# Kernel optimization log

Measured on AMD Instinct MI355X. Metric: run time of the kernel, lower is better.

The kernel has to match this reference:

```python
import jax, jax.numpy as jnp
import numpy as np

LN_EPS = 1e-5

def _layernorm(x, g, b):
    mu = jnp.mean(x, axis=-1, keepdims=True)
    var = jnp.mean(jnp.square(x - mu), axis=-1, keepdims=True)
    return (x - mu) * jax.lax.rsqrt(var + LN_EPS) * g + b

def setup_inputs() -> dict:
    key = jax.random.key(0)
    ks = jax.random.split(key, 12)
    B, S, E = 8, 4096, 512
    H, DK = 64, 8          # d_k = E // H = 8 qubits per head
    NQ_FFN, FFN = 8, 2048
    TWO_PI = 2.0 * np.pi
    x = jax.random.normal(ks[0], (B, S, E), dtype=jnp.float32)
    # trainable RX phases per attention head/wire; trainable RY phases for FFN qubits
    theta_attn = jax.random.uniform(ks[1], (H, DK), dtype=jnp.float32, maxval=TWO_PI)
    theta_ffn = jax.random.uniform(ks[2], (NQ_FFN,), dtype=jnp.float32, maxval=TWO_PI)
    s_e = 1.0 / np.sqrt(E)
    W_comb = jax.random.uniform(ks[3], (E, E), dtype=jnp.float32, minval=-s_e, maxval=s_e)
    b_comb = jax.random.uniform(ks[4], (E,), dtype=jnp.float32, minval=-s_e, maxval=s_e)
    s_q = 1.0 / np.sqrt(NQ_FFN)
    W1 = jax.random.uniform(ks[5], (FFN, NQ_FFN), dtype=jnp.float32, minval=-s_q, maxval=s_q)
    b1 = jax.random.uniform(ks[6], (FFN,), dtype=jnp.float32, minval=-s_q, maxval=s_q)
    s_f = 1.0 / np.sqrt(FFN)
    W2 = jax.random.uniform(ks[7], (E, FFN), dtype=jnp.float32, minval=-s_f, maxval=s_f)
    b2 = jax.random.uniform(ks[8], (E,), dtype=jnp.float32, minval=-s_f, maxval=s_f)
    ln1_g = jnp.ones((E,), jnp.float32); ln1_b = jnp.zeros((E,), jnp.float32)
    ln2_g = jnp.ones((E,), jnp.float32); ln2_b = jnp.zeros((E,), jnp.float32)
    return {"x": x, "theta_attn": theta_attn, "W_comb": W_comb, "b_comb": b_comb,
            "ln1_g": ln1_g, "ln1_b": ln1_b, "theta_ffn": theta_ffn,
            "W1": W1, "b1": b1, "W2": W2, "b2": b2, "ln2_g": ln2_g, "ln2_b": ln2_b}

def reference(x, theta_attn, W_comb, b_comb, ln1_g, ln1_b, theta_ffn, W1, b1, W2, b2, ln2_g, ln2_b):
    B, S, E = x.shape
    H, DK = theta_attn.shape
    NQ = theta_ffn.shape[0]
    # Quantum attention heads: RX(x) then RX(theta) on |0> per wire -> <Z> = cos(x+theta)
    q = jnp.cos(x.reshape(B, S, H, DK) + theta_attn)  # [B,S,H,DK]
    attn_out = jnp.einsum('bse,fe->bsf', q.reshape(B, S, E), W_comb) + b_comb
    x1 = _layernorm(x + attn_out, ln1_g, ln1_b)
    # Quantum FFN layer: RY(x) then RY(theta) -> <Z> = cos(x+theta), first NQ features only
    fq = jnp.cos(x1[..., :NQ] + theta_ffn)            # [B,S,NQ]
    h = jax.nn.relu(jnp.einsum('bsq,fq->bsf', fq, W1) + b1)
    ffn_out = jnp.einsum('bsf,ef->bse', h, W2) + b2
    return _layernorm(x1 + ffn_out, ln2_g, ln2_b)
```

## Files before the change

### kernel.cpp

```cpp
#include <hip/hip_runtime.h>
#include <stdint.h>

typedef unsigned short u16;
typedef __bf16 bf16x8 __attribute__((ext_vector_type(8)));
typedef float f32x4 __attribute__((ext_vector_type(4)));

#define AS1(p) ((const __attribute__((address_space(1))) void*)(p))
#define AS3(p) ((__attribute__((address_space(3))) void*)(p))

__device__ __forceinline__ float b2f(u16 v){
    union { unsigned u; float f; } x; x.u = ((unsigned)v) << 16; return x.f;
}
__device__ __forceinline__ u16 f2b(float f){
    union { float f; unsigned u; } x; x.f = f;
    unsigned r = x.u + 0x7FFFu + ((x.u >> 16) & 1u);
    return (u16)(r >> 16);
}

__global__ __launch_bounds__(256) void probe_kernel(
    const u16* p0,const u16* p1,const u16* p2,const u16* p3,const u16* p4,
    const u16* p5,const u16* p6,const u16* p7,const u16* p8,const u16* p9,
    const u16* p10,const u16* p11,const u16* p12,
    int n0,int n1,int n2,int n3,int n4,int n5,int n6,int n7,int n8,int n9,
    int n10,int n11,int n12, int* flags)
{
    const u16* p; int n;
    switch (blockIdx.x) {
        case 0: p=p0; n=n0; break;   case 1: p=p1; n=n1; break;
        case 2: p=p2; n=n2; break;   case 3: p=p3; n=n3; break;
        case 4: p=p4; n=n4; break;   case 5: p=p5; n=n5; break;
        case 6: p=p6; n=n6; break;   case 7: p=p7; n=n7; break;
        case 8: p=p8; n=n8; break;   case 9: p=p9; n=n9; break;
        case 10: p=p10; n=n10; break; case 11: p=p11; n=n11; break;
        default: p=p12; n=n12; break;
    }
    int pairs = n >> 1; if (pairs > 2048) pairs = 2048;
    int strong = 0, znz = 0, tot = 0;
    for (int k = threadIdx.x; k < pairs; k += 256) {
        u16 lo = p[2*k], hi = p[2*k+1];
        int eh = (hi >> 7) & 0xFF;
        int el = (lo >> 7) & 0xFF;
        if (eh >= 0xF0 || (eh >= 1 && eh <= 0x40)) strong = 1;
        if (el >= 0xF0 || (el >= 1 && el <= 0x40)) strong = 1;
        if (lo == 0 && hi != 0) znz++;
        tot++;
    }
    __shared__ int ss, sz, st;
    if (threadIdx.x == 0) { ss = 0; sz = 0; st = 0; }
    __syncthreads();
    if (strong) atomicOr(&ss, 1);
    if (znz) atomicAdd(&sz, znz);
    atomicAdd(&st, tot);
    __syncthreads();
    if (threadIdx.x == 0) {
        flags[blockIdx.x] = (ss || (2 * sz > st)) ? 1 : 0;
        if (blockIdx.x == 0) flags[15] = 0;
    }
}

__global__ __launch_bounds__(256) void convert_kernel(
    const void* sWc, const void* sW2, const void* sW1,
    const void* sTa, const void* sBc, const void* sG1, const void* sB1l,
    const void* sTf, const void* sB1, const void* sB2, const void* sG2, const void* sB2l,
    u16* wbase, const int* flags)
{
    int b = blockIdx.x;
    const void* src; u16* dst; int n, fi, lb, tof32 = 0;
    if (b < 128)      { src=sWc; dst=wbase;          n=262144;  fi=2;  lb=b; }
    else if (b < 640) { src=sW2; dst=wbase+262144;   n=1048576; fi=9;  lb=b-128; }
    else if (b >= 643 && b < 651) { src=sW1; dst=wbase+1312256; n=16384; fi=7; lb=b-643; }
    else {
        lb = 0;
        switch (b) {
            case 640: src=sTa;  dst=wbase+1310720; n=512;  fi=1;  break;
            case 641: src=sBc;  dst=wbase+1311232; n=512;  fi=3;  break;
            case 642: src=sB2;  dst=wbase+1311744; n=512;  fi=10; break;
            case 651: src=sB1;  dst=wbase+1328640; n=2048; fi=8;  break;
            case 652: src=sG1;  dst=wbase+1330688; n=512;  fi=4;  break;
            case 653: src=sB1l; dst=wbase+1331200; n=512;  fi=5;  break;
            case 654: src=sG2;  dst=wbase+1331712; n=512;  fi=11; break;
            case 655: src=sB2l; dst=wbase+1332224; n=512;  fi=12; break;
            default:  src=sTf;  dst=wbase+1332736; n=8;    fi=6;  tof32=1; break;
        }
    }
    int i = lb * 256 + threadIdx.x;
    if (i * 8 >= n) return;
    if (tof32) {
        float* fd = (float*)dst;
        if (flags[fi]) {
            const float4* s = (const float4*)src;
            ((float4*)fd)[i*2] = s[i*2]; ((float4*)fd)[i*2+1] = s[i*2+1];
        } else {
            union { uint4 v; u16 h[8]; } sb;
            sb.v = ((const uint4*)src)[i];
            #pragma unroll
            for (int j = 0; j < 8; j++) fd[i*8+j] = b2f(sb.h[j]);
        }
        return;
    }
    if (flags[fi]) {
        const float4* s = (const float4*)src;
        float4 a = s[i*2], c = s[i*2+1];
        union { uint4 v; u16 h[8]; } o;
        o.h[0]=f2b(a.x); o.h[1]=f2b(a.y); o.h[2]=f2b(a.z); o.h[3]=f2b(a.w);
        o.h[4]=f2b(c.x); o.h[5]=f2b(c.y); o.h[6]=f2b(c.z); o.h[7]=f2b(c.w);
        ((uint4*)dst)[i] = o.v;
    } else {
        ((uint4*)dst)[i] = ((const uint4*)src)[i];
    }
}

__global__ __launch_bounds__(256) void qgen_kernel(
    const void* __restrict__ x, const u16* __restrict__ theta,
    u16* __restrict__ q, const int* flags)
{
    const int idx = blockIdx.x * 256 + threadIdx.x;
    const int col0 = (idx * 8) & 511;
    union { uint4 v; u16 h[8]; } tb;
    tb.v = *(const uint4*)(theta + col0);
    float xv[8];
    if (flags[0]) {
        const float4* p = (const float4*)x + idx * 2;
        float4 a = p[0], b = p[1];
        xv[0]=a.x; xv[1]=a.y; xv[2]=a.z; xv[3]=a.w;
        xv[4]=b.x; xv[5]=b.y; xv[6]=b.z; xv[7]=b.w;
    } else {
        union { uint4 v; u16 h[8]; } xb;
        xb.v = ((const uint4*)x)[idx];
        #pragma unroll
        for (int e = 0; e < 8; e++) xv[e] = b2f(xb.h[e]);
    }
    union { uint4 v; u16 h[8]; } o;
    #pragma unroll
    for (int e = 0; e < 8; e++) o.h[e] = f2b(__cosf(xv[e] + b2f(tb.h[e])));
    ((uint4*)q)[idx] = o.v;
}

__global__ __launch_bounds__(256, 3) void gemm1_fused(
    const u16* __restrict__ q, const void* __restrict__ x,
    const u16* __restrict__ Wt, const u16* __restrict__ bias,
    u16* __restrict__ dst, int mtiles, const int* flags)
{
    __shared__ __align__(16) u16 As[2][128 * 64];
    __shared__ __align__(16) u16 Bs[2][128 * 64];
    const int K = 512, N = 512;
    const int tid  = threadIdx.x;
    const int lane = tid & 63;
    const int w    = tid >> 6;

    const int blk = blockIdx.x;
    const int xcd = blk & 7;
    const int j   = blk >> 3;
    const int per = mtiles >> 3;
    const int mt  = xcd * per + (j >> 2);
    const int nt  = j & 3;
    const int m0 = mt * 128;
    const int n0 = nt * 128;

    const int srow = lane >> 3;
    const int scol = ((lane & 7) ^ srow) * 8;
    const int wm = (w >> 1) * 64;
    const int wn = (w & 1) * 64;
    const int fr   = lane & 15;
    const int quad = lane >> 4;
    const int fx   = fr & 7;
    const int isf32 = flags[0];

    f32x4 acc[4][4];
    #pragma unroll
    for (int i = 0; i < 4; i++)
        #pragma unroll
        for (int jj = 0; jj < 4; jj++)
            acc[i][jj] = f32x4{0.f, 0.f, 0.f, 0.f};

    const u16* Abase = q  + (size_t)m0 * K + scol;
    const u16* Bbase = Wt + (size_t)n0 * K + scol;

    #pragma unroll
    for (int i = 0; i < 4; i++) {
        int c = w * 4 + i;
        int row = c * 8 + srow;
        __builtin_amdgcn_global_load_lds(AS1(Abase + (size_t)row * K),
                                         AS3(&As[0][c * 512]), 16, 0, 0);
        __builtin_amdgcn_global_load_lds(AS1(Bbase + (size_t)row * K),
                                         AS3(&Bs[0][c * 512]), 16, 0, 0);
    }

    int cur = 0;
    for (int kt = 0; kt < K; kt += 64) {
        __syncthreads();
        if (kt + 64 < K) {
            int nxt = cur ^ 1;
            #pragma unroll
            for (int i = 0; i < 4; i++) {
                int c = w * 4 + i;
                int row = c * 8 + srow;
                __builtin_amdgcn_global_load_lds(
                    AS1(Abase + (size_t)row * K + kt + 64),
                    AS3(&As[nxt][c * 512]), 16, 0, 0);
                __builtin_amdgcn_global_load_lds(
                    AS1(Bbase + (size_t)row * K + kt + 64),
                    AS3(&Bs[nxt][c * 512]), 16, 0, 0);
            }
        }
        #pragma unroll
        for (int kk = 0; kk < 2; kk++) {
            bf16x8 af[4], bfr[4];
            #pragma unroll
            for (int mi = 0; mi < 4; mi++)
                af[mi] = *(const bf16x8*)(&As[cur][(wm + mi * 16 + fr) * 64 +
                                          (((kk * 4 + quad) ^ fx) * 8)]);
            #pragma unroll
            for (int ni = 0; ni < 4; ni++)
                bfr[ni] = *(const bf16x8*)(&Bs[cur][(wn + ni * 16 + fr) * 64 +
                                           (((kk * 4 + quad) ^ fx) * 8)]);
            #pragma unroll
            for (int mi = 0; mi < 4; mi++)
                #pragma unroll
                for (int ni = 0; ni < 4; ni++)
                    acc[mi][ni] = __builtin_amdgcn_mfma_f32_16x16x32_bf16(
                        af[mi], bfr[ni], acc[mi][ni], 0, 0, 0);
        }
        cur ^= 1;
    }

    #pragma unroll
    for (int mi = 0; mi < 4; mi++) {
        #pragma unroll
        for (int ni = 0; ni < 4; ni++) {
            int n = n0 + wn + ni * 16 + fr;
            float bn = b2f(bias[n]);
            #pragma unroll
            for (int r = 0; r < 4; r++) {
                int m = m0 + wm + mi * 16 + quad * 4 + r;
                float rv = isf32 ? ((const float*)x)[(size_t)m * N + n]
                                 : b2f(((const u16*)x)[(size_t)m * N + n]);
                dst[(size_t)m * N + n] = f2b(acc[mi][ni][r] + bn + rv);
            }
        }
    }
}

__global__ __launch_bounds__(512, 2) void gemm2_fused(
    const u16* __restrict__ fq, const u16* __restrict__ W1, const u16* __restrict__ b1,
    const u16* __restrict__ Wt, const u16* __restrict__ bias,
    const u16* __restrict__ res, const u16* __restrict__ g2, const u16* __restrict__ b2l,
    void* __restrict__ out, const int* flags)
{
    __shared__ __align__(16) u16 Bs[2][512 * 64];
    const int K = 2048, N = 512;
    const int tid  = threadIdx.x;
    const int lane = tid & 63;
    const int w    = tid >> 6;

    const int m0 = blockIdx.x * 128;

    const int srow = lane >> 3;
    const int scol = ((lane & 7) ^ srow) * 8;
    const int wm = (w >> 2) * 64;
    const int wn = (w & 3) * 128;
    const int fr   = lane & 15;
    const int quad = lane >> 4;
    const int fx   = fr & 7;
    const int isf32 = flags[0];

    bf16x8 fqf[4];
    #pragma unroll
    for (int mi = 0; mi < 4; mi++) {
        union { uint4 v; bf16x8 b; } z; z.v = uint4{0,0,0,0};
        if (quad == 0) z.v = *(const uint4*)(fq + (size_t)(m0 + wm + mi * 16 + fr) * 8);
        fqf[mi] = z.b;
    }

    const int krow = ((fr >> 2) * 8) + (fr & 3);

    union { uint4 v; bf16x8 b; } w1f[4];
    uint2 b1f[4];
    #pragma unroll
    for (int g = 0; g < 4; g++) {
        w1f[g].v = uint4{0,0,0,0};
        if (quad == 0)
            w1f[g].v = *(const uint4*)(W1 + (size_t)((g >> 1) * 32 + (g & 1) * 4 + krow) * 8);
        b1f[g] = *(const uint2*)(b1 + (g >> 1) * 32 + (g & 1) * 4 + quad * 8);
    }

    f32x4 acc[4][8];
    #pragma unroll
    for (int i = 0; i < 4; i++)
        #pragma unroll
        for (int jj = 0; jj < 8; jj++)
            acc[i][jj] = f32x4{0.f, 0.f, 0.f, 0.f};

    const u16* Bbase = Wt + scol;
    #pragma unroll
    for (int i = 0; i < 8; i++) {
        int c = w * 8 + i;
        int row = c * 8 + srow;
        __builtin_amdgcn_global_load_lds(AS1(Bbase + (size_t)row * K),
                                         AS3(&Bs[0][c * 512]), 16, 0, 0);
    }

    int cur = 0;
    for (int kt = 0; kt < K; kt += 64) {
        __syncthreads();
        if (kt + 64 < K) {
            int nxt = cur ^ 1;
            #pragma unroll
            for (int i = 0; i < 8; i++) {
                int c = w * 8 + i;
                int row = c * 8 + srow;
                __builtin_amdgcn_global_load_lds(
                    AS1(Bbase + (size_t)row * K + kt + 64),
                    AS3(&Bs[nxt][c * 512]), 16, 0, 0);
            }
        }
        #pragma unroll
        for (int kk = 0; kk < 2; kk++) {
            const u16* pb0 = (const u16*)&b1f[kk * 2 + 0];
            const u16* pb1 = (const u16*)&b1f[kk * 2 + 1];
            f32x4 c0 = {b2f(pb0[0]), b2f(pb0[1]), b2f(pb0[2]), b2f(pb0[3])};
            f32x4 c1 = {b2f(pb1[0]), b2f(pb1[1]), b2f(pb1[2]), b2f(pb1[3])};
            bf16x8 af[4];
            #pragma unroll
            for (int mi = 0; mi < 4; mi++) {
                f32x4 hv0 = __builtin_amdgcn_mfma_f32_16x16x32_bf16(
                    w1f[kk * 2 + 0].b, fqf[mi], c0, 0, 0, 0);
                f32x4 hv1 = __builtin_amdgcn_mfma_f32_16x16x32_bf16(
                    w1f[kk * 2 + 1].b, fqf[mi], c1, 0, 0, 0);
                #pragma unroll
                for (int r = 0; r < 4; r++) {
                    af[mi][r]     = (__bf16)fmaxf(hv0[r], 0.f);
                    af[mi][4 + r] = (__bf16)fmaxf(hv1[r], 0.f);
                }
            }
            #pragma unroll
            for (int np = 0; np < 4; np++) {
                bf16x8 bfr[2];
                #pragma unroll
                for (int ni = 0; ni < 2; ni++)
                    bfr[ni] = *(const bf16x8*)(&Bs[cur][(wn + (np * 2 + ni) * 16 + fr) * 64 +
                                               (((kk * 4 + quad) ^ fx) * 8)]);
                #pragma unroll
                for (int mi = 0; mi < 4; mi++)
                    #pragma unroll
                    for (int ni = 0; ni < 2; ni++)
                        acc[mi][np * 2 + ni] = __builtin_amdgcn_mfma_f32_16x16x32_bf16(
                            af[mi], bfr[ni], acc[mi][np * 2 + ni], 0, 0, 0);
            }
        }
        if (kt + 64 < K) {
            #pragma unroll
            for (int g = 0; g < 4; g++) {
                if (quad == 0)
                    w1f[g].v = *(const uint4*)(W1 +
                        (size_t)(kt + 64 + (g >> 1) * 32 + (g & 1) * 4 + krow) * 8);
                b1f[g] = *(const uint2*)(b1 + kt + 64 + (g >> 1) * 32 + (g & 1) * 4 + quad * 8);
            }
        }
        cur ^= 1;
    }

    __syncthreads();
    u16* zt = &Bs[0][0];
    #pragma unroll
    for (int mi = 0; mi < 4; mi++) {
        #pragma unroll
        for (int nq = 0; nq < 8; nq++) {
            int n = wn + nq * 16 + fr;
            float bn = b2f(bias[n]);
            #pragma unroll
            for (int r = 0; r < 4; r++) {
                int lm = wm + mi * 16 + quad * 4 + r;
                float v = acc[mi][nq][r] + bn + b2f(res[(size_t)(m0 + lm) * N + n]);
                zt[lm * 512 + n] = f2b(v);
            }
        }
    }
    __syncthreads();

    {
        union { uint4 v; u16 s[8]; } gb, bb;
        gb.v = *(const uint4*)(g2 + lane * 8);
        bb.v = *(const uint4*)(b2l + lane * 8);
        for (int i = 0; i < 16; i++) {
            int row = w * 16 + i;
            union { uint4 v; u16 s[8]; } zb;
            zb.v = ((const uint4*)(zt + row * 512))[lane];
            float xv[8], s = 0.f, ss = 0.f;
            #pragma unroll
            for (int jj = 0; jj < 8; jj++) {
                xv[jj] = b2f(zb.s[jj]); s += xv[jj]; ss += xv[jj] * xv[jj];
            }
            #pragma unroll
            for (int o = 32; o > 0; o >>= 1) { s += __shfl_down(s, o); ss += __shfl_down(ss, o); }
            s = __shfl(s, 0); ss = __shfl(ss, 0);
            float mu = s * (1.f / 512.f);
            float rs = rsqrtf(ss * (1.f / 512.f) - mu * mu + 1e-5f);
            size_t m = (size_t)(m0 + row);
            if (isf32) {
                float xn[8];
                #pragma unroll
                for (int jj = 0; jj < 8; jj++)
                    xn[jj] = (xv[jj] - mu) * rs * b2f(gb.s[jj]) + b2f(bb.s[jj]);
                float* po = (float*)out + m * N + lane * 8;
                *(float4*)po       = float4{xn[0], xn[1], xn[2], xn[3]};
                *(float4*)(po + 4) = float4{xn[4], xn[5], xn[6], xn[7]};
            } else {
                union { uint4 v; u16 s[8]; } ob;
                #pragma unroll
                for (int jj = 0; jj < 8; jj++)
                    ob.s[jj] = f2b((xv[jj] - mu) * rs * b2f(gb.s[jj]) + b2f(bb.s[jj]));
                ((uint4*)((u16*)out + m * N))[lane] = ob.v;
            }
        }
    }
}

__global__ __launch_bounds__(512) void ln1_kernel(
    const u16* __restrict__ y1, const u16* __restrict__ g, const u16* __restrict__ b,
    const float* __restrict__ tf, u16* __restrict__ x1, u16* __restrict__ fqout)
{
    __shared__ __align__(16) float xs8[64][8];
    const int t = threadIdx.x;
    const int wv = t >> 6, l = t & 63;
    const size_t rbase = (size_t)blockIdx.x * 64;

    union { uint4 v; u16 s[8]; } gb, bb;
    gb.v = *(const uint4*)(g + l * 8);
    bb.v = *(const uint4*)(b + l * 8);

    #pragma unroll
    for (int i = 0; i < 8; i++) {
        int lr = wv * 8 + i;
        union { uint4 v; u16 s[8]; } yb;
        yb.v = ((const uint4*)(y1 + (rbase + lr) * 512))[l];
        float xv[8], s = 0.f, ss = 0.f;
        #pragma unroll
        for (int jj = 0; jj < 8; jj++) {
            xv[jj] = b2f(yb.s[jj]); s += xv[jj]; ss += xv[jj] * xv[jj];
        }
        #pragma unroll
        for (int o = 32; o > 0; o >>= 1) { s += __shfl_down(s, o); ss += __shfl_down(ss, o); }
        s = __shfl(s, 0); ss = __shfl(ss, 0);
        float mu = s * (1.f / 512.f);
        float rs = rsqrtf(ss * (1.f / 512.f) - mu * mu + 1e-5f);
        union { uint4 v; u16 s[8]; } ob;
        float xn[8];
        #pragma unroll
        for (int jj = 0; jj < 8; jj++) {
            xn[jj] = (xv[jj] - mu) * rs * b2f(gb.s[jj]) + b2f(bb.s[jj]);
            ob.s[jj] = f2b(xn[jj]);
        }
        ((uint4*)(x1 + (rbase + lr) * 512))[l] = ob.v;
        if (l == 0) {
            #pragma unroll
            for (int jj = 0; jj < 8; jj++) xs8[lr][jj] = xn[jj];
        }
    }
    __syncthreads();
    {
        int r = t >> 3, jj = t & 7;
        fqout[(rbase + r) * 8 + jj] = f2b(__cosf(xs8[r][jj] + tf[jj]));
    }
}

extern "C" void kernel_launch(void* const* d_in, const int* in_sizes, int n_in,
                              void* d_out, int out_size, void* d_ws, size_t ws_size,
                              hipStream_t stream)
{
    u16* ws16 = (u16*)d_ws;
    u16* W     = ws16;
    int* flags = (int*)(ws16 + 1332752);
    u16* fq  = ws16 + 1332800;
    u16* x1  = ws16 + 1594944;
    u16* q   = x1;
    u16* y1  = ws16 + 18372160;

    const u16*  wWc  = W;
    const u16*  wW2  = W + 262144;
    const u16*  wTa  = W + 1310720;
    const u16*  wBc  = W + 1311232;
    const u16*  wB2  = W + 1311744;
    const u16*  wW1  = W + 1312256;
    const u16*  wB1  = W + 1328640;
    const u16*  wG1  = W + 1330688;
    const u16*  wB1l = W + 1331200;
    const u16*  wG2  = W + 1331712;
    const u16*  wB2l = W + 1332224;
    const float* wTf = (const float*)(W + 1332736);

    probe_kernel<<<13, 256, 0, stream>>>(
        (const u16*)d_in[0], (const u16*)d_in[1], (const u16*)d_in[2],
        (const u16*)d_in[3], (const u16*)d_in[4], (const u16*)d_in[5],
        (const u16*)d_in[6], (const u16*)d_in[7], (const u16*)d_in[8],
        (const u16*)d_in[9], (const u16*)d_in[10], (const u16*)d_in[11],
        (const u16*)d_in[12],
        in_sizes[0], in_sizes[1], in_sizes[2], in_sizes[3], in_sizes[4],
        in_sizes[5], in_sizes[6], in_sizes[7], in_sizes[8], in_sizes[9],
        in_sizes[10], in_sizes[11], in_sizes[12], flags);

    convert_kernel<<<657, 256, 0, stream>>>(
        d_in[2], d_in[9], d_in[7], d_in[1], d_in[3], d_in[4], d_in[5],
        d_in[6], d_in[8], d_in[10], d_in[11], d_in[12], (u16*)W, flags);

    qgen_kernel<<<8192, 256, 0, stream>>>(d_in[0], wTa, q, flags);

    gemm1_fused<<<1024, 256, 0, stream>>>(
        q, d_in[0], wWc, wBc, y1, 256, flags);

    ln1_kernel<<<512, 512, 0, stream>>>(y1, wG1, wB1l, wTf, x1, fq);

    gemm2_fused<<<256, 512, 0, stream>>>(
        fq, wW1, wB1, wW2, wB2, x1, wG2, wB2l, d_out, flags);
}
```

Measured before the change: 306.3 us.

## Fuse LayerNorm1 and FFN quantum features into full-row GEMM1 epilogue

GEMM1 now computes a full 128x512 output row tile per block (512 threads, whole W_comb tile staged in LDS), stages the residual-added result in shared memory, then performs LayerNorm1 and the cos feature computation in-block. This removes the separate ln1 kernel and the y1 intermediate round trip through global memory. In exchange the grid shrinks from 1024 to 256 blocks with more LDS per block, which lowers parallelism and occupancy. x1 also aliases q, and each block reads only its own q rows before writing its own x1 rows, so the in-place write looks safe.

Result: no change. 301.3 us (-1.6%).

```diff
diff --git a/kernel.cpp b/kernel.cpp
--- a/kernel.cpp
+++ b/kernel.cpp
@@ -136,52 +136,52 @@
     ((uint4*)q)[idx] = o.v;
 }
 
-__global__ __launch_bounds__(256, 3) void gemm1_fused(
-    const u16* __restrict__ q, const void* __restrict__ x,
+__global__ __launch_bounds__(512, 2) void gemm1_fused(
+    const u16* q, const void* __restrict__ x,
     const u16* __restrict__ Wt, const u16* __restrict__ bias,
-    u16* __restrict__ dst, int mtiles, const int* flags)
+    const u16* __restrict__ g1, const u16* __restrict__ b1l,
+    const float* __restrict__ tf,
+    u16* x1out, u16* __restrict__ fqout, const int* flags)
 {
     __shared__ __align__(16) u16 As[2][128 * 64];
-    __shared__ __align__(16) u16 Bs[2][128 * 64];
+    __shared__ __align__(16) u16 Bs[2][512 * 64];
     const int K = 512, N = 512;
     const int tid  = threadIdx.x;
     const int lane = tid & 63;
     const int w    = tid >> 6;
 
-    const int blk = blockIdx.x;
-    const int xcd = blk & 7;
-    const int j   = blk >> 3;
-    const int per = mtiles >> 3;
-    const int mt  = xcd * per + (j >> 2);
-    const int nt  = j & 3;
-    const int m0 = mt * 128;
-    const int n0 = nt * 128;
+    const int m0 = blockIdx.x * 128;
 
     const int srow = lane >> 3;
     const int scol = ((lane & 7) ^ srow) * 8;
-    const int wm = (w >> 1) * 64;
-    const int wn = (w & 1) * 64;
+    const int wm = (w >> 2) * 64;
+    const int wn = (w & 3) * 128;
     const int fr   = lane & 15;
     const int quad = lane >> 4;
     const int fx   = fr & 7;
     const int isf32 = flags[0];
 
-    f32x4 acc[4][4];
+    f32x4 acc[4][8];
     #pragma unroll
     for (int i = 0; i < 4; i++)
         #pragma unroll
-        for (int jj = 0; jj < 4; jj++)
+        for (int jj = 0; jj < 8; jj++)
             acc[i][jj] = f32x4{0.f, 0.f, 0.f, 0.f};
 
     const u16* Abase = q  + (size_t)m0 * K + scol;
-    const u16* Bbase = Wt + (size_t)n0 * K + scol;
-
-    #pragma unroll
-    for (int i = 0; i < 4; i++) {
-        int c = w * 4 + i;
+    const u16* Bbase = Wt + scol;
+
+    #pragma unroll
+    for (int i = 0; i < 2; i++) {
+        int c = w * 2 + i;
         int row = c * 8 + srow;
         __builtin_amdgcn_global_load_lds(AS1(Abase + (size_t)row * K),
                                          AS3(&As[0][c * 512]), 16, 0, 0);
+    }
+    #pragma unroll
+    for (int i = 0; i < 8; i++) {
+        int c = w * 8 + i;
+        int row = c * 8 + srow;
         __builtin_amdgcn_global_load_lds(AS1(Bbase + (size_t)row * K),
                                          AS3(&Bs[0][c * 512]), 16, 0, 0);
     }
@@ -192,12 +192,17 @@
         if (kt + 64 < K) {
             int nxt = cur ^ 1;
             #pragma unroll
-            for (int i = 0; i < 4; i++) {
-                int c = w * 4 + i;
+            for (int i = 0; i < 2; i++) {
+                int c = w * 2 + i;
                 int row = c * 8 + srow;
                 __builtin_amdgcn_global_load_lds(
                     AS1(Abase + (size_t)row * K + kt + 64),
                     AS3(&As[nxt][c * 512]), 16, 0, 0);
+            }
+            #pragma unroll
+            for (int i = 0; i < 8; i++) {
+                int c = w * 8 + i;
+                int row = c * 8 + srow;
                 __builtin_amdgcn_global_load_lds(
                     AS1(Bbase + (size_t)row * K + kt + 64),
                     AS3(&Bs[nxt][c * 512]), 16, 0, 0);
@@ -205,37 +210,78 @@
         }
         #pragma unroll
         for (int kk = 0; kk < 2; kk++) {
-            bf16x8 af[4], bfr[4];
+            bf16x8 af[4];
             #pragma unroll
             for (int mi = 0; mi < 4; mi++)
                 af[mi] = *(const bf16x8*)(&As[cur][(wm + mi * 16 + fr) * 64 +
                                           (((kk * 4 + quad) ^ fx) * 8)]);
             #pragma unroll
-            for (int ni = 0; ni < 4; ni++)
-                bfr[ni] = *(const bf16x8*)(&Bs[cur][(wn + ni * 16 + fr) * 64 +
-                                           (((kk * 4 + quad) ^ fx) * 8)]);
-            #pragma unroll
-            for (int mi = 0; mi < 4; mi++)
-                #pragma unroll
-                for (int ni = 0; ni < 4; ni++)
-                    acc[mi][ni] = __builtin_amdgcn_mfma_f32_16x16x32_bf16(
-                        af[mi], bfr[ni], acc[mi][ni], 0, 0, 0);
+            for (int np = 0; np < 4; np++) {
+                bf16x8 bfr[2];
+                #pragma unroll
+                for (int ni = 0; ni < 2; ni++)
+                    bfr[ni] = *(const bf16x8*)(&Bs[cur][(wn + (np * 2 + ni) * 16 + fr) * 64 +
+                                               (((kk * 4 + quad) ^ fx) * 8)]);
+                #pragma unroll
+                for (int mi = 0; mi < 4; mi++)
+                    #pragma unroll
+                    for (int ni = 0; ni < 2; ni++)
+                        acc[mi][np * 2 + ni] = __builtin_amdgcn_mfma_f32_16x16x32_bf16(
+                            af[mi], bfr[ni], acc[mi][np * 2 + ni], 0, 0, 0);
+            }
         }
         cur ^= 1;
     }
 
+    __syncthreads();
+    u16* zt = &Bs[0][0];
     #pragma unroll
     for (int mi = 0; mi < 4; mi++) {
         #pragma unroll
-        for (int ni = 0; ni < 4; ni++) {
-            int n = n0 + wn + ni * 16 + fr;
+        for (int nq = 0; nq < 8; nq++) {
+            int n = wn + nq * 16 + fr;
             float bn = b2f(bias[n]);
             #pragma unroll
             for (int r = 0; r < 4; r++) {
-                int m = m0 + wm + mi * 16 + quad * 4 + r;
-                float rv = isf32 ? ((const float*)x)[(size_t)m * N + n]
-                                 : b2f(((const u16*)x)[(size_t)m * N + n]);
-                dst[(size_t)m * N + n] = f2b(acc[mi][ni][r] + bn + rv);
+                int lm = wm + mi * 16 + quad * 4 + r;
+                float rv = isf32 ? ((const float*)x)[(size_t)(m0 + lm) * N + n]
+                                 : b2f(((const u16*)x)[(size_t)(m0 + lm) * N + n]);
+                zt[lm * 512 + n] = f2b(acc[mi][nq][r] + bn + rv);
+            }
+        }
+    }
+    __syncthreads();
+
+    {
+        union { uint4 v; u16 s[8]; } gb, bb;
+        gb.v = *(const uint4*)(g1 + lane * 8);
+        bb.v = *(const uint4*)(b1l + lane * 8);
+        for (int i = 0; i < 16; i++) {
+            int row = w * 16 + i;
+            union { uint4 v; u16 s[8]; } zb;
+            zb.v = ((const uint4*)(zt + row * 512))[lane];
+            float xv[8], s = 0.f, ss = 0.f;
+            #pragma unroll
+            for (int jj = 0; jj < 8; jj++) {
+                xv[jj] = b2f(zb.s[jj]); s += xv[jj]; ss += xv[jj] * xv[jj];
+            }
+            #pragma unroll
+            for (int o = 32; o > 0; o >>= 1) { s += __shfl_down(s, o); ss += __shfl_down(ss, o); }
+            s = __shfl(s, 0); ss = __shfl(ss, 0);
+            float mu = s * (1.f / 512.f);
+            float rs = rsqrtf(ss * (1.f / 512.f) - mu * mu + 1e-5f);
+            float xn[8];
+            union { uint4 v; u16 s[8]; } ob;
+            #pragma unroll
+            for (int jj = 0; jj < 8; jj++) {
+                xn[jj] = (xv[jj] - mu) * rs * b2f(gb.s[jj]) + b2f(bb.s[jj]);
+                ob.s[jj] = f2b(xn[jj]);
+            }
+            ((uint4*)(x1out + (size_t)(m0 + row) * 512))[lane] = ob.v;
+            if (lane == 0) {
+                #pragma unroll
+                for (int jj = 0; jj < 8; jj++)
+                    fqout[(size_t)(m0 + row) * 8 + jj] = f2b(__cosf(xn[jj] + tf[jj]));
             }
         }
     }
@@ -416,54 +462,6 @@
     }
 }
 
-__global__ __launch_bounds__(512) void ln1_kernel(
-    const u16* __restrict__ y1, const u16* __restrict__ g, const u16* __restrict__ b,
-    const float* __restrict__ tf, u16* __restrict__ x1, u16* __restrict__ fqout)
-{
-    __shared__ __align__(16) float xs8[64][8];
-    const int t = threadIdx.x;
-    const int wv = t >> 6, l = t & 63;
-    const size_t rbase = (size_t)blockIdx.x * 64;
-
-    union { uint4 v; u16 s[8]; } gb, bb;
-    gb.v = *(const uint4*)(g + l * 8);
-    bb.v = *(const uint4*)(b + l * 8);
-
-    #pragma unroll
-    for (int i = 0; i < 8; i++) {
-        int lr = wv * 8 + i;
-        union { uint4 v; u16 s[8]; } yb;
-        yb.v = ((const uint4*)(y1 + (rbase + lr) * 512))[l];
-        float xv[8], s = 0.f, ss = 0.f;
-        #pragma unroll
-        for (int jj = 0; jj < 8; jj++) {
-            xv[jj] = b2f(yb.s[jj]); s += xv[jj]; ss += xv[jj] * xv[jj];
-        }
-        #pragma unroll
-        for (int o = 32; o > 0; o >>= 1) { s += __shfl_down(s, o); ss += __shfl_down(ss, o); }
-        s = __shfl(s, 0); ss = __shfl(ss, 0);
-        float mu = s * (1.f / 512.f);
-        float rs = rsqrtf(ss * (1.f / 512.f) - mu * mu + 1e-5f);
-        union { uint4 v; u16 s[8]; } ob;
-        float xn[8];
-        #pragma unroll
-        for (int jj = 0; jj < 8; jj++) {
-            xn[jj] = (xv[jj] - mu) * rs * b2f(gb.s[jj]) + b2f(bb.s[jj]);
-            ob.s[jj] = f2b(xn[jj]);
-        }
-        ((uint4*)(x1 + (rbase + lr) * 512))[l] = ob.v;
-        if (l == 0) {
-            #pragma unroll
-            for (int jj = 0; jj < 8; jj++) xs8[lr][jj] = xn[jj];
-        }
-    }
-    __syncthreads();
-    {
-        int r = t >> 3, jj = t & 7;
-        fqout[(rbase + r) * 8 + jj] = f2b(__cosf(xs8[r][jj] + tf[jj]));
-    }
-}
-
 extern "C" void kernel_launch(void* const* d_in, const int* in_sizes, int n_in,
                               void* d_out, int out_size, void* d_ws, size_t ws_size,
                               hipStream_t stream)
@@ -474,7 +472,6 @@
     u16* fq  = ws16 + 1332800;
     u16* x1  = ws16 + 1594944;
     u16* q   = x1;
-    u16* y1  = ws16 + 18372160;
 
     const u16*  wWc  = W;
     const u16*  wW2  = W + 262144;
@@ -505,10 +502,8 @@
 
     qgen_kernel<<<8192, 256, 0, stream>>>(d_in[0], wTa, q, flags);
 
-    gemm1_fused<<<1024, 256, 0, stream>>>(
-        q, d_in[0], wWc, wBc, y1, 256, flags);
-
-    ln1_kernel<<<512, 512, 0, stream>>>(y1, wG1, wB1l, wTf, x1, fq);
+    gemm1_fused<<<256, 512, 0, stream>>>(
+        q, d_in[0], wWc, wBc, wG1, wB1l, wTf, x1, fq, flags);
 
     gemm2_fused<<<256, 512, 0, stream>>>(
         fq, wW1, wB1, wW2, wB2, x1, wG2, wB2l, d_out, flags);
```
